# Kernel optimization log

Hardware: AMD Instinct MI355X
Metric: run time of the kernel (lower is better)

The kernel has to match this reference:

```python
import jax, jax.numpy as jnp
import numpy as np

# dims (must match input_specs / init_kwargs)
B, N, L, D = 4, 2000, 32, 64
H, ND, K, DOUT = 4, 64, 20, 64  # num_heads, node_dim, topk, out_dim
EPS = 1e-8


def setup_inputs() -> dict:
    key = jax.random.key(0)
    ks = jax.random.split(key, 10)
    lim_emb = float(np.sqrt(6.0 / (N + ND)))  # xavier_uniform-ish for embeddings
    lim_l1 = float(np.sqrt(1.0 / H))          # torch Linear default-ish
    lim_l2 = float(np.sqrt(1.0 / (2 * H)))
    lim_w = float(np.sqrt(6.0 / (D + DOUT)))
    return {
        "x": jax.random.normal(ks[0], (B, N, L, D), dtype=jnp.float32),
        "e1": jax.random.uniform(ks[1], (H, N, ND), minval=-lim_emb, maxval=lim_emb, dtype=jnp.float32),
        "e2": jax.random.uniform(ks[2], (H, ND, N), minval=-lim_emb, maxval=lim_emb, dtype=jnp.float32),
        "temperature": jnp.ones((H,), dtype=jnp.float32),
        "ew1": jax.random.uniform(ks[3], (H, 2 * H), minval=-lim_l1, maxval=lim_l1, dtype=jnp.float32),
        "eb1": jax.random.uniform(ks[4], (2 * H,), minval=-lim_l1, maxval=lim_l1, dtype=jnp.float32),
        "ew2": jax.random.uniform(ks[5], (2 * H, 1), minval=-lim_l2, maxval=lim_l2, dtype=jnp.float32),
        "eb2": jax.random.uniform(ks[6], (1,), minval=-lim_l2, maxval=lim_l2, dtype=jnp.float32),
        "weight": jax.random.uniform(ks[7], (D, DOUT), minval=-lim_w, maxval=lim_w, dtype=jnp.float32),
        "bias": jnp.zeros((DOUT,), dtype=jnp.float32),
    }


def _graph_learner(e1, e2, temperature, ew1, eb1, ew2, eb2):
    # per-head scores: (H, N, N)
    scores = jnp.einsum("hnd,hdm->hnm", e1, e2)
    adj = jax.nn.softmax(jax.nn.relu(scores) / temperature[:, None, None], axis=-1)
    # topk sparsification along each row (dim=1 in torch == last axis here)
    _, idx = jax.lax.top_k(adj, K)  # (H, N, K)
    mask = jnp.zeros_like(adj).at[
        jnp.arange(H)[:, None, None], jnp.arange(N)[None, :, None], idx
    ].set(1.0)
    adj = adj * mask
    adj = adj / (jnp.sum(adj, axis=-1, keepdims=True) + EPS)
    # edge encoder MLP over head dim (dropout is identity in eval mode)
    feats = jnp.transpose(adj, (1, 2, 0))              # (N, N, H)
    hid = jax.nn.relu(feats @ ew1 + eb1)               # (N, N, 2H)
    ew = (hid @ ew2 + eb2)[..., 0]                     # (N, N)
    final_adj = jax.nn.sigmoid(ew) * jnp.mean(adj, axis=0)
    return final_adj, adj


def reference(x, e1, e2, temperature, ew1, eb1, ew2, eb2, weight, bias):
    final_adj, _ = _graph_learner(e1, e2, temperature, ew1, eb1, ew2, eb2)
    Bv, Nv, Lv, Dv = x.shape
    xr = jnp.transpose(x, (0, 2, 1, 3)).reshape(Bv * Lv, Nv, Dv)  # (B*L, N, D)
    support = xr @ weight                                          # (B*L, N, Dout)
    # adj.t() @ support  ->  out[b,i,:] = sum_j adj[j,i] * support[b,j,:]
    out = jnp.einsum("ji,bjd->bid", final_adj, support) + bias
    out = jnp.transpose(out.reshape(Bv, Lv, Nv, -1), (0, 2, 1, 3))  # (B, N, L, Dout)
    return out, final_adj
```

## Files before the change

kernel.cpp:

```cpp
#include <hip/hip_runtime.h>

#define NB   2000
#define HH   4
#define KK   20
#define KP   2048
#define GA   4
#define EPSF 1e-8f

typedef unsigned short ushort;
typedef unsigned long long ull;
using short8   = __attribute__((ext_vector_type(8))) short;
using floatx4  = __attribute__((ext_vector_type(4))) float;
using ushortx4 = __attribute__((ext_vector_type(4))) unsigned short;
using ushortx8 = __attribute__((ext_vector_type(8))) unsigned short;

__device__ inline ushort f2bf(float f) {
    unsigned u = __builtin_bit_cast(unsigned, f);
    u += 0x7fffu + ((u >> 16) & 1u);
    return (ushort)(u >> 16);
}

__device__ __forceinline__ void gload_lds16(const ushort* g, ushort* l) {
    __builtin_amdgcn_global_load_lds(
        (const __attribute__((address_space(1))) void*)g,
        (__attribute__((address_space(3))) void*)l, 16, 0, 0);
}

template<int CTRL>
__device__ __forceinline__ float dppmax(float x) {
    int xi = __builtin_bit_cast(int, x);
    int yi = __builtin_amdgcn_update_dpp(xi, xi, CTRL, 0xF, 0xF, false);
    return fmaxf(x, __builtin_bit_cast(float, yi));
}

__device__ __forceinline__ float wavemax63(float x) {
    x = dppmax<0x111>(x);
    x = dppmax<0x112>(x);
    x = dppmax<0x114>(x);
    x = dppmax<0x118>(x);
    x = dppmax<0x142>(x);
    x = dppmax<0x143>(x);
    return x;
}

#define COMP(v,i) ((i)==0?(v).x:(i)==1?(v).y:(i)==2?(v).z:(v).w)

__global__ __launch_bounds__(512) void k_scores_topk(
    const float* __restrict__ e1, const float* __restrict__ e2,
    const float* __restrict__ temperature,
    int* __restrict__ topk_idx, float* __restrict__ topk_val)
{
    const int h  = blockIdx.y;
    const int n0 = blockIdx.x * GA;
    const int t  = threadIdx.x;
    const int w  = t >> 6, lane = t & 63;

    __shared__ float e1s[GA][64];
    __shared__ float scoresS[GA][2048];
    __shared__ float red[GA][4];
    __shared__ ull   lists[4][GA][KK + 1];
    __shared__ float selpv[GA][KK];
    __shared__ int   seli[GA][KK];
    __shared__ float ssum[GA];

    if (t < 256)
        e1s[t >> 6][t & 63] = e1[(size_t)(h * NB + n0 + (t >> 6)) * 64 + (t & 63)];
    __syncthreads();

    const float rtemp = 1.f / temperature[h];
    const float* __restrict__ e2h = e2 + (size_t)h * 64 * NB;

    {
        const int mb1 = w * 256 + lane * 4;
        const int ml1 = (mb1 < NB) ? mb1 : (NB - 4);

        float acc[GA][4];
#pragma unroll
        for (int r = 0; r < GA; r++)
#pragma unroll
            for (int c = 0; c < 4; c++) acc[r][c] = 0.f;

        for (int d4 = 0; d4 < 64; d4 += 4) {
            float4 ev0 = *(const float4*)&e1s[0][d4];
            float4 ev1 = *(const float4*)&e1s[1][d4];
            float4 ev2 = *(const float4*)&e1s[2][d4];
            float4 ev3 = *(const float4*)&e1s[3][d4];
#pragma unroll
            for (int dd = 0; dd < 4; dd++) {
                float4 a = *(const float4*)(e2h + (size_t)(d4 + dd) * NB + ml1);
                float f0 = COMP(ev0, dd), f1 = COMP(ev1, dd);
                float f2 = COMP(ev2, dd), f3 = COMP(ev3, dd);
                acc[0][0] += f0*a.x; acc[0][1] += f0*a.y; acc[0][2] += f0*a.z; acc[0][3] += f0*a.w;
                acc[1][0] += f1*a.x; acc[1][1] += f1*a.y; acc[1][2] += f1*a.z; acc[1][3] += f1*a.w;
                acc[2][0] += f2*a.x; acc[2][1] += f2*a.y; acc[2][2] += f2*a.z; acc[2][3] += f2*a.w;
                acc[3][0] += f3*a.x; acc[3][1] += f3*a.y; acc[3][2] += f3*a.z; acc[3][3] += f3*a.w;
            }
        }

#pragma unroll
        for (int r = 0; r < GA; r++) {
            float4 v; v.x = acc[r][0]; v.y = acc[r][1]; v.z = acc[r][2]; v.w = acc[r][3];
            *(float4*)&scoresS[r][mb1] = v;
        }
    }
    __syncthreads();

    if (w < 4) {
        const int  mbase = w * 512 + lane * 8;
        const bool valid = (mbase < NB);

        float acc[GA][8];
#pragma unroll
        for (int r = 0; r < GA; r++) {
            float4 lo = *(const float4*)&scoresS[r][mbase];
            float4 hi = *(const float4*)&scoresS[r][mbase + 4];
            acc[r][0] = lo.x; acc[r][1] = lo.y; acc[r][2] = lo.z; acc[r][3] = lo.w;
            acc[r][4] = hi.x; acc[r][5] = hi.y; acc[r][6] = hi.z; acc[r][7] = hi.w;
        }

#pragma unroll
        for (int r = 0; r < GA; r++) {
            float tvm = -1.f;
#pragma unroll
            for (int k = 0; k < 8; k++) {
                float v = valid ? fmaxf(acc[r][k], 0.f) * rtemp : -1.f;
                acc[r][k] = v;
                tvm = fmaxf(tvm, v);
            }
            tvm = wavemax63(tvm);
            if (lane == 63) red[r][w] = tvm;
        }

        float lm[GA]; int ak[GA];
#pragma unroll
        for (int r = 0; r < GA; r++) {
            float l = acc[r][0]; int a = 0;
#pragma unroll
            for (int k = 1; k < 8; k++)
                if (acc[r][k] > l) { l = acc[r][k]; a = k; }
            lm[r] = l; ak[r] = a;
        }

        for (int round = 0; round < KK; round++) {
            float M[GA];
#pragma unroll
            for (int r = 0; r < GA; r++) M[r] = lm[r];
#pragma unroll
            for (int r = 0; r < GA; r++) M[r] = dppmax<0x111>(M[r]);
#pragma unroll
            for (int r = 0; r < GA; r++) M[r] = dppmax<0x112>(M[r]);
#pragma unroll
            for (int r = 0; r < GA; r++) M[r] = dppmax<0x114>(M[r]);
#pragma unroll
            for (int r = 0; r < GA; r++) M[r] = dppmax<0x118>(M[r]);
#pragma unroll
            for (int r = 0; r < GA; r++) M[r] = dppmax<0x142>(M[r]);
#pragma unroll
            for (int r = 0; r < GA; r++) M[r] = dppmax<0x143>(M[r]);
#pragma unroll
            for (int r = 0; r < GA; r++)
                M[r] = __builtin_bit_cast(float,
                         __builtin_amdgcn_readlane(__builtin_bit_cast(int, M[r]), 63));
#pragma unroll
            for (int r = 0; r < GA; r++) {
                ull ball = __ballot(lm[r] == M[r]);
                int wl   = __ffsll(ball) - 1;
                if (lane == wl) {
                    int gidx = mbase + ak[r];
                    lists[w][r][round] =
                        ((ull)__float_as_uint(M[r]) << 32) | (unsigned)~gidx;
#pragma unroll
                    for (int k = 0; k < 8; k++) if (k == ak[r]) acc[r][k] = -2.f;
                    float l = acc[r][0]; int a = 0;
#pragma unroll
                    for (int k = 1; k < 8; k++)
                        if (acc[r][k] > l) { l = acc[r][k]; a = k; }
                    lm[r] = l; ak[r] = a;
                }
            }
        }
#pragma unroll
        for (int r = 0; r < GA; r++)
            if (lane == 0) lists[w][r][KK] = 0ULL;
    }
    __syncthreads();

    if (t < GA) {
        const int r = t;
        float mx = fmaxf(fmaxf(red[r][0], red[r][1]), fmaxf(red[r][2], red[r][3]));
        int p0 = 0, p1 = 0, p2 = 0, p3 = 0;
        ull h0 = lists[0][r][0], h1 = lists[1][r][0];
        ull h2 = lists[2][r][0], h3 = lists[3][r][0];
        float ss = 0.f;
        for (int q = 0; q < KK; q++) {
            ull a_ = h0 >= h1 ? h0 : h1; int wa = h0 >= h1 ? 0 : 1;
            ull b_ = h2 >= h3 ? h2 : h3; int wb = h2 >= h3 ? 2 : 3;
            ull bk = a_ >= b_ ? a_ : b_; int bw = a_ >= b_ ? wa : wb;
            float tvv = __uint_as_float((unsigned)(bk >> 32));
            float pv  = __expf(tvv - mx);
            selpv[r][q] = pv;
            seli[r][q]  = (int)~(unsigned)bk;
            ss += pv;
            if      (bw == 0) h0 = lists[0][r][++p0];
            else if (bw == 1) h1 = lists[1][r][++p1];
            else if (bw == 2) h2 = lists[2][r][++p2];
            else              h3 = lists[3][r][++p3];
        }
        ssum[r] = ss;
    }
    __syncthreads();

    if (t < GA * KK) {
        int r = t / KK, q = t % KK;
        int o = (h * NB + n0 + r) * KK + q;
        topk_idx[o] = seli[r][q];
        topk_val[o] = selpv[r][q] / (ssum[r] + EPSF);
    }
}

__global__ __launch_bounds__(256) void k_final_adj(
    const int* __restrict__ topk_idx, const float* __restrict__ topk_val,
    const float* __restrict__ ew1, const float* __restrict__ eb1,
    const float* __restrict__ ew2, const float* __restrict__ eb2,
    float* __restrict__ fadj_out, ushort* __restrict__ faT_b)
{
    const int i = blockIdx.x;
    const int t = threadIdx.x;

    __shared__ float rows[HH][NB];
    __shared__ float w1[32];
    __shared__ float b1[8];
    __shared__ float w2[8];
    __shared__ float b2v;

    for (int k = t; k < HH * NB; k += 256) ((float*)rows)[k] = 0.f;
    if (t < 32) w1[t] = ew1[t];
    if (t < 8)  { b1[t] = eb1[t]; w2[t] = ew2[t]; }
    if (t == 0) b2v = eb2[0];
    __syncthreads();

    if (t < HH * KK) {
        int h = t / KK, r = t % KK;
        int o = (h * NB + i) * KK + r;
        rows[h][topk_idx[o]] = topk_val[o];
    }
    __syncthreads();

#pragma unroll
    for (int k = 0; k < 8; k++) {
        int j = k * 256 + t;
        if (j < NB) {
            float f0 = rows[0][j], f1 = rows[1][j], f2 = rows[2][j], f3 = rows[3][j];
            float mean = (f0 + f1 + f2 + f3) * 0.25f;
            float outv = 0.f;
            if (mean > 0.f) {
                float ewv = b2v;
#pragma unroll
                for (int c = 0; c < 8; c++) {
                    float hid = f0 * w1[c] + f1 * w1[8 + c] + f2 * w1[16 + c] + f3 * w1[24 + c] + b1[c];
                    hid = fmaxf(hid, 0.f);
                    ewv += hid * w2[c];
                }
                float sig = 1.f / (1.f + expf(-ewv));
                outv = sig * mean;
                faT_b[(size_t)j * KP + i] = f2bf(outv);
            }
            fadj_out[(size_t)i * NB + j] = outv;
        }
    }
}

__global__ __launch_bounds__(256) void k_support(
    const float* __restrict__ x, const float* __restrict__ w,
    ushort* __restrict__ S_b)
{
    const int j = blockIdx.x;
    const int t = threadIdx.x;

    __shared__ float xs[128 * 65];
    __shared__ float ws[64 * 64];

    for (int k = t; k < 4096; k += 256) ws[k] = w[k];
    for (int idx = t; idx < 8192; idx += 256) {
        int b_ = idx >> 11, rem = idx & 2047;
        int bl = (b_ << 5) + (rem >> 6), dd = rem & 63;
        xs[bl * 65 + dd] = x[(size_t)b_ * 4096000 + (size_t)j * 2048 + rem];
    }
    __syncthreads();

    const int dq = t & 15;
    const int g  = t >> 4;
    float acc[8][4];
#pragma unroll
    for (int r = 0; r < 8; r++)
#pragma unroll
        for (int c = 0; c < 4; c++) acc[r][c] = 0.f;

    for (int dd = 0; dd < 64; dd++) {
        float4 w4 = *(const float4*)&ws[dd * 64 + dq * 4];
#pragma unroll
        for (int r = 0; r < 8; r++) {
            float xv = xs[(g * 8 + r) * 65 + dd];
            acc[r][0] += xv * w4.x;
            acc[r][1] += xv * w4.y;
            acc[r][2] += xv * w4.z;
            acc[r][3] += xv * w4.w;
        }
    }

#pragma unroll
    for (int r = 0; r < 8; r++) {
        int bl = g * 8 + r;
        ushortx4 v;
        v.x = f2bf(acc[r][0]); v.y = f2bf(acc[r][1]);
        v.z = f2bf(acc[r][2]); v.w = f2bf(acc[r][3]);
        *(ushortx4*)&S_b[(size_t)j * 8192 + bl * 64 + dq * 4] = v;
    }
}

__global__ __launch_bounds__(256) void k_transpose(
    const ushort* __restrict__ S_b, ushort* __restrict__ ST)
{
    const int jt = blockIdx.x;
    const int ct = blockIdx.y;
    const int t  = threadIdx.x;

    __shared__ ushort tile[64 * 65];

#pragma unroll
    for (int p = 0; p < 4; p++) {
        int q = p * 256 + t;
        int row = q >> 4, seg = q & 15;
        int j = jt * 64 + row;
        ushort v0 = 0, v1 = 0, v2 = 0, v3 = 0;
        if (j < NB) {
            const ushort* src = &S_b[(size_t)j * 8192 + ct * 64 + seg * 4];
            v0 = src[0]; v1 = src[1]; v2 = src[2]; v3 = src[3];
        }
        ushort* dst = &tile[row * 65 + seg * 4];
        dst[0] = v0; dst[1] = v1; dst[2] = v2; dst[3] = v3;
    }
    __syncthreads();

#pragma unroll
    for (int p = 0; p < 2; p++) {
        int q = p * 256 + t;
        int rc = q >> 3, s = q & 7;
        ushortx8 o;
#pragma unroll
        for (int k = 0; k < 8; k++) o[k] = tile[(s * 8 + k) * 65 + rc];
        *(ushortx8*)&ST[(size_t)(ct * 64 + rc) * KP + jt * 64 + s * 8] = o;
    }
}

__global__ __launch_bounds__(256) void k_gemm(
    const ushort* __restrict__ A, const ushort* __restrict__ B,
    const float* __restrict__ bias, float* __restrict__ out)
{
    __shared__ ushort As[128 * 64];
    __shared__ ushort Bs[128 * 64];

    const int t    = threadIdx.x;
    const int lane = t & 63, wave = t >> 6;
    const int wm   = wave & 1, wn = wave >> 1;
    const int i0   = blockIdx.x * 128;
    const int c0   = blockIdx.y * 128;

    const int lr = lane >> 3;
    const int dg = lane & 7;

    floatx4 acc[4][4];
#pragma unroll
    for (int r = 0; r < 4; r++)
#pragma unroll
        for (int c = 0; c < 4; c++) acc[r][c] = (floatx4)(0.f);

    for (int kb = 0; kb < 32; kb++) {
        __syncthreads();
#pragma unroll
        for (int p = 0; p < 4; p++) {
            int rowb = p * 32 + wave * 8;
            int row  = rowb + lr;
            int g    = dg ^ lr;
            const ushort* ga = &A[(size_t)(i0 + row) * KP + kb * 64 + g * 8];
            const ushort* gb = &B[(size_t)(c0 + row) * KP + kb * 64 + g * 8];
            gload_lds16(ga, &As[rowb * 64]);
            gload_lds16(gb, &Bs[rowb * 64]);
        }
        __syncthreads();

#pragma unroll
        for (int kk = 0; kk < 2; kk++) {
            short8 af[4], bf[4];
            const int gidx = kk * 4 + (lane >> 4);
            const int dsw  = gidx ^ (lane & 7);
#pragma unroll
            for (int r = 0; r < 4; r++) {
                int m = wm * 64 + r * 16 + (lane & 15);
                af[r] = *(const short8*)&As[m * 64 + dsw * 8];
            }
#pragma unroll
            for (int c = 0; c < 4; c++) {
                int m = wn * 64 + c * 16 + (lane & 15);
                bf[c] = *(const short8*)&Bs[m * 64 + dsw * 8];
            }
#pragma unroll
            for (int r = 0; r < 4; r++)
#pragma unroll
                for (int c = 0; c < 4; c++)
                    acc[r][c] = __builtin_amdgcn_mfma_f32_16x16x32_bf16(af[r], bf[c], acc[r][c], 0, 0, 0);
        }
    }

    const int mq = (lane >> 4) * 4;
    const int nn = lane & 15;
#pragma unroll
    for (int r = 0; r < 4; r++) {
#pragma unroll
        for (int c = 0; c < 4; c++) {
            int cg = c0 + wn * 64 + c * 16 + nn;
            float bv = bias[cg & 63];
            int b_ = cg >> 11, rem = cg & 2047;
            float* op = out + (size_t)b_ * 4096000 + rem;
#pragma unroll
            for (int rg = 0; rg < 4; rg++) {
                int i = i0 + wm * 64 + r * 16 + mq + rg;
                if (i < NB) op[(size_t)i * 2048] = acc[r][c][rg] + bv;
            }
        }
    }
}

extern "C" void kernel_launch(void* const* d_in, const int* in_sizes, int n_in,
                              void* d_out, int out_size, void* d_ws, size_t ws_size,
                              hipStream_t stream)
{
    const float* x           = (const float*)d_in[0];
    const float* e1          = (const float*)d_in[1];
    const float* e2          = (const float*)d_in[2];
    const float* temperature = (const float*)d_in[3];
    const float* ew1         = (const float*)d_in[4];
    const float* eb1         = (const float*)d_in[5];
    const float* ew2         = (const float*)d_in[6];
    const float* eb2         = (const float*)d_in[7];
    const float* weight      = (const float*)d_in[8];
    const float* bias        = (const float*)d_in[9];

    float* out  = (float*)d_out;
    float* fadj = out + 16384000;

    ushort* ST       = (ushort*)d_ws;
    ushort* S_b      = ST + (size_t)8192 * KP;
    ushort* faT_b    = (ushort*)((char*)d_ws + 66322432u);
    int*    topk_idx = (int*)(faT_b + (size_t)KP * KP);
    float*  topk_val = (float*)(topk_idx + 160000);

    hipMemsetAsync(faT_b, 0, (size_t)KP * KP * sizeof(ushort), stream);

    k_scores_topk<<<dim3(NB / GA, HH), 512, 0, stream>>>(e1, e2, temperature,
                                                         topk_idx, topk_val);
    k_final_adj<<<NB, 256, 0, stream>>>(topk_idx, topk_val, ew1, eb1, ew2, eb2,
                                        fadj, faT_b);
    k_support<<<NB, 256, 0, stream>>>(x, weight, S_b);
    k_transpose<<<dim3(32, 128), 256, 0, stream>>>(S_b, ST);
    k_gemm<<<dim3(16, 64), 256, 0, stream>>>(faT_b, ST, bias, out);
}
```

Before: 393.8 us.

## Process sixteen score rows per block with 1024 threads in scores/top-k kernel

The scores/top-k kernel now handles 16 rows of a head per block instead of 4, using 1024 threads. Each e2 load is reused across 16 rows rather than 4, and all 16 waves take part in the top-k selection phase (four rows per group of four waves) instead of half the waves sitting idle. In exchange, shared memory per block grows to roughly 145 KB, so only one block fits per CU. The grid drops to 500 blocks, and the launch bound of (1024, 2) plus 16 float4 e1 values per thread raises register pressure and the risk of spills.

```diff
diff --git a/kernel.cpp b/kernel.cpp
--- a/kernel.cpp
+++ b/kernel.cpp
@@ -4,7 +4,7 @@
 #define HH   4
 #define KK   20
 #define KP   2048
-#define GA   4
+#define GR   16
 #define EPSF 1e-8f
 
 typedef unsigned short ushort;
@@ -45,81 +45,80 @@
 
 #define COMP(v,i) ((i)==0?(v).x:(i)==1?(v).y:(i)==2?(v).z:(v).w)
 
-__global__ __launch_bounds__(512) void k_scores_topk(
+__global__ __launch_bounds__(1024, 2) void k_scores_topk(
     const float* __restrict__ e1, const float* __restrict__ e2,
     const float* __restrict__ temperature,
     int* __restrict__ topk_idx, float* __restrict__ topk_val)
 {
     const int h  = blockIdx.y;
-    const int n0 = blockIdx.x * GA;
+    const int n0 = blockIdx.x * GR;
     const int t  = threadIdx.x;
     const int w  = t >> 6, lane = t & 63;
 
-    __shared__ float e1s[GA][64];
-    __shared__ float scoresS[GA][2048];
-    __shared__ float red[GA][4];
-    __shared__ ull   lists[4][GA][KK + 1];
-    __shared__ float selpv[GA][KK];
-    __shared__ int   seli[GA][KK];
-    __shared__ float ssum[GA];
-
-    if (t < 256)
-        e1s[t >> 6][t & 63] = e1[(size_t)(h * NB + n0 + (t >> 6)) * 64 + (t & 63)];
+    __shared__ float e1s[GR][64];
+    __shared__ float scoresS[GR][2048];
+    __shared__ float red[GR][4];
+    __shared__ ull   lists[4][GR][KK + 1];
+    __shared__ float selpv[GR][KK];
+    __shared__ int   seli[GR][KK];
+    __shared__ float ssum[GR];
+
+    e1s[t >> 6][t & 63] = e1[(size_t)(h * NB + n0 + (t >> 6)) * 64 + (t & 63)];
     __syncthreads();
 
     const float rtemp = 1.f / temperature[h];
     const float* __restrict__ e2h = e2 + (size_t)h * 64 * NB;
 
     {
-        const int mb1 = w * 256 + lane * 4;
-        const int ml1 = (mb1 < NB) ? mb1 : (NB - 4);
-
-        float acc[GA][4];
-#pragma unroll
-        for (int r = 0; r < GA; r++)
-#pragma unroll
-            for (int c = 0; c < 4; c++) acc[r][c] = 0.f;
-
+        const int mb1 = w * 128 + lane * 2;
+        const int ml1 = (mb1 < NB) ? mb1 : (NB - 2);
+
+        float acc[GR][2];
+#pragma unroll
+        for (int r = 0; r < GR; r++) { acc[r][0] = 0.f; acc[r][1] = 0.f; }
+
+#pragma unroll 2
         for (int d4 = 0; d4 < 64; d4 += 4) {
-            float4 ev0 = *(const float4*)&e1s[0][d4];
-            float4 ev1 = *(const float4*)&e1s[1][d4];
-            float4 ev2 = *(const float4*)&e1s[2][d4];
-            float4 ev3 = *(const float4*)&e1s[3][d4];
+            float4 ev[GR];
+#pragma unroll
+            for (int r = 0; r < GR; r++) ev[r] = *(const float4*)&e1s[r][d4];
 #pragma unroll
             for (int dd = 0; dd < 4; dd++) {
-                float4 a = *(const float4*)(e2h + (size_t)(d4 + dd) * NB + ml1);
-                float f0 = COMP(ev0, dd), f1 = COMP(ev1, dd);
-                float f2 = COMP(ev2, dd), f3 = COMP(ev3, dd);
-                acc[0][0] += f0*a.x; acc[0][1] += f0*a.y; acc[0][2] += f0*a.z; acc[0][3] += f0*a.w;
-                acc[1][0] += f1*a.x; acc[1][1] += f1*a.y; acc[1][2] += f1*a.z; acc[1][3] += f1*a.w;
-                acc[2][0] += f2*a.x; acc[2][1] += f2*a.y; acc[2][2] += f2*a.z; acc[2][3] += f2*a.w;
-                acc[3][0] += f3*a.x; acc[3][1] += f3*a.y; acc[3][2] += f3*a.z; acc[3][3] += f3*a.w;
-            }
-        }
-
-#pragma unroll
-        for (int r = 0; r < GA; r++) {
-            float4 v; v.x = acc[r][0]; v.y = acc[r][1]; v.z = acc[r][2]; v.w = acc[r][3];
-            *(float4*)&scoresS[r][mb1] = v;
-        }
-    }
-    __syncthreads();
-
-    if (w < 4) {
-        const int  mbase = w * 512 + lane * 8;
+                float2 a = *(const float2*)(e2h + (size_t)(d4 + dd) * NB + ml1);
+#pragma unroll
+                for (int r = 0; r < GR; r++) {
+                    float f = COMP(ev[r], dd);
+                    acc[r][0] += f * a.x;
+                    acc[r][1] += f * a.y;
+                }
+            }
+        }
+
+#pragma unroll
+        for (int r = 0; r < GR; r++) {
+            float2 v; v.x = acc[r][0]; v.y = acc[r][1];
+            *(float2*)&scoresS[r][mb1] = v;
+        }
+    }
+    __syncthreads();
+
+    {
+        const int hw = w >> 2;
+        const int sl = w & 3;
+        const int  mbase = sl * 512 + lane * 8;
         const bool valid = (mbase < NB);
 
-        float acc[GA][8];
-#pragma unroll
-        for (int r = 0; r < GA; r++) {
-            float4 lo = *(const float4*)&scoresS[r][mbase];
-            float4 hi = *(const float4*)&scoresS[r][mbase + 4];
+        float acc[4][8];
+#pragma unroll
+        for (int r = 0; r < 4; r++) {
+            float4 lo = *(const float4*)&scoresS[hw * 4 + r][mbase];
+            float4 hi = *(const float4*)&scoresS[hw * 4 + r][mbase + 4];
             acc[r][0] = lo.x; acc[r][1] = lo.y; acc[r][2] = lo.z; acc[r][3] = lo.w;
             acc[r][4] = hi.x; acc[r][5] = hi.y; acc[r][6] = hi.z; acc[r][7] = hi.w;
         }
 
 #pragma unroll
-        for (int r = 0; r < GA; r++) {
+        for (int r = 0; r < 4; r++) {
             float tvm = -1.f;
 #pragma unroll
             for (int k = 0; k < 8; k++) {
@@ -128,12 +127,12 @@
                 tvm = fmaxf(tvm, v);
             }
             tvm = wavemax63(tvm);
-            if (lane == 63) red[r][w] = tvm;
-        }
-
-        float lm[GA]; int ak[GA];
-#pragma unroll
-        for (int r = 0; r < GA; r++) {
+            if (lane == 63) red[hw * 4 + r][sl] = tvm;
+        }
+
+        float lm[4]; int ak[4];
+#pragma unroll
+        for (int r = 0; r < 4; r++) {
             float l = acc[r][0]; int a = 0;
 #pragma unroll
             for (int k = 1; k < 8; k++)
@@ -142,32 +141,32 @@
         }
 
         for (int round = 0; round < KK; round++) {
-            float M[GA];
-#pragma unroll
-            for (int r = 0; r < GA; r++) M[r] = lm[r];
-#pragma unroll
-            for (int r = 0; r < GA; r++) M[r] = dppmax<0x111>(M[r]);
-#pragma unroll
-            for (int r = 0; r < GA; r++) M[r] = dppmax<0x112>(M[r]);
-#pragma unroll
-            for (int r = 0; r < GA; r++) M[r] = dppmax<0x114>(M[r]);
-#pragma unroll
-            for (int r = 0; r < GA; r++) M[r] = dppmax<0x118>(M[r]);
-#pragma unroll
-            for (int r = 0; r < GA; r++) M[r] = dppmax<0x142>(M[r]);
-#pragma unroll
-            for (int r = 0; r < GA; r++) M[r] = dppmax<0x143>(M[r]);
-#pragma unroll
-            for (int r = 0; r < GA; r++)
+            float M[4];
+#pragma unroll
+            for (int r = 0; r < 4; r++) M[r] = lm[r];
+#pragma unroll
+            for (int r = 0; r < 4; r++) M[r] = dppmax<0x111>(M[r]);
+#pragma unroll
+            for (int r = 0; r < 4; r++) M[r] = dppmax<0x112>(M[r]);
+#pragma unroll
+            for (int r = 0; r < 4; r++) M[r] = dppmax<0x114>(M[r]);
+#pragma unroll
+            for (int r = 0; r < 4; r++) M[r] = dppmax<0x118>(M[r]);
+#pragma unroll
+            for (int r = 0; r < 4; r++) M[r] = dppmax<0x142>(M[r]);
+#pragma unroll
+            for (int r = 0; r < 4; r++) M[r] = dppmax<0x143>(M[r]);
+#pragma unroll
+            for (int r = 0; r < 4; r++)
                 M[r] = __builtin_bit_cast(float,
                          __builtin_amdgcn_readlane(__builtin_bit_cast(int, M[r]), 63));
 #pragma unroll
-            for (int r = 0; r < GA; r++) {
+            for (int r = 0; r < 4; r++) {
                 ull ball = __ballot(lm[r] == M[r]);
                 int wl   = __ffsll(ball) - 1;
                 if (lane == wl) {
                     int gidx = mbase + ak[r];
-                    lists[w][r][round] =
+                    lists[sl][hw * 4 + r][round] =
                         ((ull)__float_as_uint(M[r]) << 32) | (unsigned)~gidx;
 #pragma unroll
                     for (int k = 0; k < 8; k++) if (k == ak[r]) acc[r][k] = -2.f;
@@ -180,12 +179,12 @@
             }
         }
 #pragma unroll
-        for (int r = 0; r < GA; r++)
-            if (lane == 0) lists[w][r][KK] = 0ULL;
-    }
-    __syncthreads();
-
-    if (t < GA) {
+        for (int r = 0; r < 4; r++)
+            if (lane == 0) lists[sl][hw * 4 + r][KK] = 0ULL;
+    }
+    __syncthreads();
+
+    if (t < GR) {
         const int r = t;
         float mx = fmaxf(fmaxf(red[r][0], red[r][1]), fmaxf(red[r][2], red[r][3]));
         int p0 = 0, p1 = 0, p2 = 0, p3 = 0;
@@ -210,7 +209,7 @@
     }
     __syncthreads();
 
-    if (t < GA * KK) {
+    if (t < GR * KK) {
         int r = t / KK, q = t % KK;
         int o = (h * NB + n0 + r) * KK + q;
         topk_idx[o] = seli[r][q];
@@ -457,8 +456,8 @@
 
     hipMemsetAsync(faT_b, 0, (size_t)KP * KP * sizeof(ushort), stream);
 
-    k_scores_topk<<<dim3(NB / GA, HH), 512, 0, stream>>>(e1, e2, temperature,
-                                                         topk_idx, topk_val);
+    k_scores_topk<<<dim3(NB / GR, HH), 1024, 0, stream>>>(e1, e2, temperature,
+                                                          topk_idx, topk_val);
     k_final_adj<<<NB, 256, 0, stream>>>(topk_idx, topk_val, ew1, eb1, ew2, eb2,
                                         fadj, faT_b);
     k_support<<<NB, 256, 0, stream>>>(x, weight, S_b);
```

After: 404.5 us. 2.7% more time.
